# Optimization experiments

Measured on AMD Instinct MI355X. Metric: run time of the kernel, lower is better.

The kernel has to match this reference:

```python
import jax, jax.numpy as jnp
import numpy as np

TEMPERATURE = 0.2
NUM_CLASSES = 80  # background label == NUM_CLASSES
M, K, B = 8192, 128, 60


def setup_inputs() -> dict:
    key = jax.random.key(0)
    k1, k2, k3 = jax.random.split(key, 3)
    feats = jax.random.normal(k1, (M, K), dtype=jnp.float32)
    feats = feats / jnp.linalg.norm(feats, axis=-1, keepdims=True)
    protos = jax.random.normal(k2, (B, K), dtype=jnp.float32)
    protos = protos / jnp.linalg.norm(protos, axis=-1, keepdims=True)
    labels = jax.random.randint(k3, (M,), 0, NUM_CLASSES + 1)  # NUM_CLASSES == bg
    proto_labels = jnp.arange(B, dtype=jnp.int64 if jax.config.read('jax_enable_x64') else jnp.int32)
    return {"features": feats, "labels": labels, "protos": protos, "proto_labels": proto_labels}


def reference(features, labels, protos, proto_labels):
    # masked (fixed-shape) formulation of the original boolean-gather code
    fg = labels != NUM_CLASSES                                   # [M]
    is_base = fg & jnp.any(labels[None, :] == proto_labels[:, None], axis=0)
    is_novel = fg & ~is_base
    nf = is_novel.astype(features.dtype)                         # [M] novel mask
    bf = is_base.astype(features.dtype)                          # [M] base mask
    numel = jnp.sum(fg).astype(features.dtype)

    sim = jnp.matmul(features, features.T) / TEMPERATURE          # [M,M]
    pk = jnp.matmul(features, protos.T) / TEMPERATURE             # [M,B]
    exp_sim = jnp.exp(sim)                                        # [M,M]
    eye = jnp.eye(features.shape[0], dtype=features.dtype)
    offdiag = (1.0 - eye)

    # ---- novel branch: rows i with is_novel[i] ----
    # denom: sum over novel j != i of exp(sim) + sum over protos of RAW pk (faithful to source)
    exp_nn_sum = jnp.sum(exp_sim * nf[None, :] * offdiag, axis=1)  # [M]
    denom_n = exp_nn_sum + jnp.sum(pk, axis=1)                     # [M]
    log_prob = sim - jnp.log(denom_n)[:, None]
    # novel_label_mask in source is elementwise labels==labels -> all True
    n_novel = jnp.sum(nf)
    cnt = jnp.maximum(n_novel - 1.0, 1.0)                          # per-row positive count
    per_row_novel = -jnp.sum(log_prob * nf[None, :] * offdiag, axis=1) / cnt
    loss_novel = jnp.sum(per_row_novel * nf)
    loss_novel = jnp.where(n_novel > 1.0, loss_novel, 0.0)

    # ---- base branch: rows i with is_base[i] ----
    safe_lab = jnp.clip(labels, 0, protos.shape[0] - 1)
    pi = jnp.einsum('nc,nc->n', features, protos[safe_lab]) / TEMPERATURE  # [M]
    denom_b = jnp.sum(exp_sim * nf[None, :], axis=1) + jnp.sum(jnp.exp(pk), axis=1)
    loss_base = jnp.sum(bf * -(pi - jnp.log(denom_b)))
    loss_base = jnp.where(jnp.any(is_base), loss_base, 0.0)

    return (loss_novel + loss_base) / numel
```

## Files before the change

kernel.cpp:

```cpp
#include <hip/hip_runtime.h>
#include <math.h>

#define NCLS 80
#define KDIM 128
#define INV_T 5.0f
#define AST 136
#define BST 72

typedef __attribute__((ext_vector_type(4))) float  floatx4;
typedef __attribute__((ext_vector_type(8))) short  short8;

__device__ inline unsigned short f2bf(float x) {
    unsigned int u = __float_as_uint(x);
    u += 0x7fffu + ((u >> 16) & 1u);
    return (unsigned short)(u >> 16);
}
__device__ inline ushort4 pack4(float4 v) {
    ushort4 r; r.x = f2bf(v.x); r.y = f2bf(v.y); r.z = f2bf(v.z); r.w = f2bf(v.w);
    return r;
}

__global__ __launch_bounds__(256) void setup_kernel(
    const int* __restrict__ labels, int M, int B,
    int* __restrict__ novel_idx, int* __restrict__ counters,
    float* __restrict__ S1, float* __restrict__ T1,
    float* __restrict__ PKr, float* __restrict__ EK, float* __restrict__ out)
{
    int i = blockIdx.x * 256 + threadIdx.x;
    if (i == 0) out[0] = 0.f;
    if (i >= M) return;
    S1[i] = 0.f; T1[i] = 0.f; PKr[i] = 0.f; EK[i] = 0.f;
    int lab = labels[i];
    bool fg  = (lab != NCLS);
    bool isb = fg && (lab >= 0) && (lab < B);
    bool isn = fg && !isb;
    if (isn) { int p = atomicAdd(&counters[0], 1); novel_idx[p] = i; }
    if (fg)  atomicAdd(&counters[1], 1);
    if (isb) atomicAdd(&counters[2], 1);
}

__global__ __launch_bounds__(256, 2) void gemm_kernel(
    const float* __restrict__ feats, const float* __restrict__ protos,
    const int* __restrict__ novel_idx, const int* __restrict__ counters,
    int M, int B,
    float* __restrict__ S1, float* __restrict__ T1,
    float* __restrict__ PKr, float* __restrict__ EK)
{
    __shared__ unsigned short As[128 * AST];
    __shared__ unsigned short Bs[128 * BST];
    __shared__ int nidx[128];

    const int Nn = counters[0];
    const int ntiles = (Nn + 127) >> 7;
    const int ct = blockIdx.x >> 6;
    const int rt = blockIdx.x & 63;
    if (ct > ntiles) return;
    const bool isproto = (ct == ntiles);
    const int row0 = rt * 128;
    const int tid = threadIdx.x;

    {
        const float4* f4 = (const float4*)(feats + (size_t)row0 * KDIM);
        #pragma unroll
        for (int p = 0; p < 16; ++p) {
            int chunk = p * 256 + tid;
            int r = chunk >> 5, kc = chunk & 31;
            float4 v = f4[r * 32 + kc];
            *(ushort4*)&As[r * AST + kc * 4] = pack4(v);
        }
    }

    const int wave = tid >> 6;
    const int lane = tid & 63;
    const int lr   = lane & 15;
    const int quad = lane >> 4;
    const int wrow = (wave >> 1) * 64;
    const int wcol = (wave & 1) * 64;

    floatx4 acc[4][4];
    #pragma unroll
    for (int r = 0; r < 4; ++r)
        #pragma unroll
        for (int c = 0; c < 4; ++c)
            acc[r][c] = (floatx4){0.f, 0.f, 0.f, 0.f};

    for (int h = 0; h < 2; ++h) {
        if (h) __syncthreads();
        #pragma unroll
        for (int p = 0; p < 8; ++p) {
            int chunk = p * 256 + tid;
            int r = chunk >> 4, kc = chunk & 15;
            float4 v = make_float4(0.f, 0.f, 0.f, 0.f);
            if (isproto) {
                if (r < B) v = *(const float4*)(protos + (size_t)r * KDIM + h * 64 + kc * 4);
            } else {
                int jg = ct * 128 + r;
                if (jg < Nn) {
                    int nid = novel_idx[jg];
                    v = *(const float4*)(feats + (size_t)nid * KDIM + h * 64 + kc * 4);
                }
            }
            *(ushort4*)&Bs[r * BST + kc * 4] = pack4(v);
        }
        if (h == 0 && tid < 128) {
            int nid = -1;
            if (isproto) { if (tid < B) nid = tid; }
            else { int jg = ct * 128 + tid; if (jg < Nn) nid = novel_idx[jg]; }
            nidx[tid] = nid;
        }
        __syncthreads();
        #pragma unroll
        for (int ks = 0; ks < 2; ++ks) {
            short8 a[4], b[4];
            #pragma unroll
            for (int r = 0; r < 4; ++r)
                a[r] = *(const short8*)&As[(wrow + r * 16 + lr) * AST + h * 64 + ks * 32 + quad * 8];
            #pragma unroll
            for (int c = 0; c < 4; ++c)
                b[c] = *(const short8*)&Bs[(wcol + c * 16 + lr) * BST + ks * 32 + quad * 8];
            #pragma unroll
            for (int r = 0; r < 4; ++r)
                #pragma unroll
                for (int c = 0; c < 4; ++c)
                    acc[r][c] = __builtin_amdgcn_mfma_f32_16x16x32_bf16(
                        a[r], b[c], acc[r][c], 0, 0, 0);
        }
    }

    int ncol[4];
    #pragma unroll
    for (int c = 0; c < 4; ++c) ncol[c] = nidx[wcol + c * 16 + lr];

    #pragma unroll
    for (int r = 0; r < 4; ++r) {
        int ibase = row0 + wrow + r * 16 + quad * 4;
        #pragma unroll
        for (int reg = 0; reg < 4; ++reg) {
            int irow = ibase + reg;
            float se = 0.f, sr = 0.f;
            #pragma unroll
            for (int c = 0; c < 4; ++c) {
                float sim = acc[r][c][reg] * INV_T;
                bool valid = (ncol[c] >= 0) && (isproto || ncol[c] != irow);
                if (valid) { se += __expf(sim); sr += sim; }
            }
            #pragma unroll
            for (int off = 1; off < 16; off <<= 1) {
                se += __shfl_xor(se, off);
                sr += __shfl_xor(sr, off);
            }
            if (lr == 0) {
                if (isproto) { atomicAdd(&EK[irow], se); atomicAdd(&PKr[irow], sr); }
                else         { atomicAdd(&S1[irow], se); atomicAdd(&T1[irow], sr); }
            }
        }
    }
}

__global__ __launch_bounds__(256) void finalize_kernel(
    const float* __restrict__ feats, const float* __restrict__ protos,
    const int* __restrict__ labels,
    const float* __restrict__ S1, const float* __restrict__ T1,
    const float* __restrict__ PKr, const float* __restrict__ EK,
    const int* __restrict__ counters, int M, int B, float* __restrict__ out)
{
    __shared__ float part[16];
    const int tid  = threadIdx.x;
    const int rloc = tid >> 4;
    const int q    = tid & 15;
    const int row  = blockIdx.x * 16 + rloc;
    const int rs   = min(row, M - 1);

    const int Nn = counters[0], numel = counters[1], nbase = counters[2];

    int lab = labels[rs];
    bool fg  = (lab != NCLS);
    bool isb = fg && (lab >= 0) && (lab < B);
    bool isn = fg && !isb;
    int  sl  = min(max(lab, 0), B - 1);

    float d = 0.f;
    #pragma unroll
    for (int j = 0; j < 8; ++j) {
        int k = q + j * 16;
        d += feats[(size_t)rs * KDIM + k] * protos[(size_t)sl * KDIM + k];
    }
    #pragma unroll
    for (int off = 1; off < 16; off <<= 1) d += __shfl_xor(d, off);

    if (q == 0) {
        float loss = 0.f;
        if (row < M) {
            if (isn && Nn > 1) {
                float cnt = (float)(Nn - 1);
                float dn  = S1[rs] + PKr[rs];
                loss = -(T1[rs] - cnt * logf(dn)) / cnt;
            } else if (isb && nbase > 0) {
                float pi = d * INV_T;
                float db = S1[rs] + EK[rs];
                loss = -(pi - logf(db));
            }
        }
        part[rloc] = loss;
    }
    __syncthreads();
    if (tid == 0) {
        float s = 0.f;
        #pragma unroll
        for (int r = 0; r < 16; ++r) s += part[r];
        atomicAdd(out, s / (float)numel);
    }
}

extern "C" void kernel_launch(void* const* d_in, const int* in_sizes, int n_in,
                              void* d_out, int out_size, void* d_ws, size_t ws_size,
                              hipStream_t stream)
{
    const float* feats  = (const float*)d_in[0];
    const int*   labels = (const int*)d_in[1];
    const float* protos = (const float*)d_in[2];

    const int M = in_sizes[1];
    const int B = in_sizes[3];

    char* ws = (char*)d_ws;
    int*   counters  = (int*)ws;
    float* S1  = (float*)(ws + 64);
    float* T1  = S1 + M;
    float* PKr = T1 + M;
    float* EK  = PKr + M;
    int*   novel_idx = (int*)(EK + M);

    hipMemsetAsync(counters, 0, 64, stream);

    setup_kernel<<<(M + 255) / 256, 256, 0, stream>>>(
        labels, M, B, novel_idx, counters, S1, T1, PKr, EK, (float*)d_out);

    int rowTiles = (M + 127) / 128;
    int maxct    = (M + 127) / 128;
    gemm_kernel<<<rowTiles * (maxct + 1), 256, 0, stream>>>(
        feats, protos, novel_idx, counters, M, B, S1, T1, PKr, EK);

    finalize_kernel<<<(M + 15) / 16, 256, 0, stream>>>(
        feats, protos, labels, S1, T1, PKr, EK, counters, M, B, (float*)d_out);
}
```

Measured before the change: 107.5 us.

## Pre-convert features to bf16 once and stream tiles via direct global-to-LDS loads

The setup kernel now converts all feature and prototype rows to bf16 once into workspace, including a zero pad row used for out-of-range novel columns. The GEMM kernel then fills its A and B tiles with global_load_lds 16-byte transfers into an XOR-swizzled LDS layout instead of per-block fp32 loads and conversions. The full K=128 tile is loaded at once with a single barrier. This removes repeated fp32 reads and conversions that every column tile did for the same rows. In exchange it adds a bf16 copy to workspace, a larger LDS footprint (64KB), and a dependency on the swizzle matching the lane-address layout of global_load_lds.

```diff
diff --git a/kernel.cpp b/kernel.cpp
--- a/kernel.cpp
+++ b/kernel.cpp
@@ -4,8 +4,6 @@
 #define NCLS 80
 #define KDIM 128
 #define INV_T 5.0f
-#define AST 136
-#define BST 72
 
 typedef __attribute__((ext_vector_type(4))) float  floatx4;
 typedef __attribute__((ext_vector_type(8))) short  short8;
@@ -15,39 +13,69 @@
     u += 0x7fffu + ((u >> 16) & 1u);
     return (unsigned short)(u >> 16);
 }
-__device__ inline ushort4 pack4(float4 v) {
-    ushort4 r; r.x = f2bf(v.x); r.y = f2bf(v.y); r.z = f2bf(v.z); r.w = f2bf(v.w);
-    return r;
+__device__ inline short8 pack8(float4 a, float4 b) {
+    short8 o;
+    o[0] = (short)f2bf(a.x); o[1] = (short)f2bf(a.y);
+    o[2] = (short)f2bf(a.z); o[3] = (short)f2bf(a.w);
+    o[4] = (short)f2bf(b.x); o[5] = (short)f2bf(b.y);
+    o[6] = (short)f2bf(b.z); o[7] = (short)f2bf(b.w);
+    return o;
+}
+__device__ inline void g2lds16(const void* g, void* l) {
+    __builtin_amdgcn_global_load_lds(
+        (const __attribute__((address_space(1))) void*)g,
+        (__attribute__((address_space(3))) void*)l, 16, 0, 0);
 }
 
 __global__ __launch_bounds__(256) void setup_kernel(
-    const int* __restrict__ labels, int M, int B,
+    const float* __restrict__ feats, const int* __restrict__ labels,
+    const float* __restrict__ protos, int M, int B,
     int* __restrict__ novel_idx, int* __restrict__ counters,
     float* __restrict__ S1, float* __restrict__ T1,
-    float* __restrict__ PKr, float* __restrict__ EK, float* __restrict__ out)
-{
-    int i = blockIdx.x * 256 + threadIdx.x;
+    float* __restrict__ PKr, float* __restrict__ EK, float* __restrict__ out,
+    unsigned short* __restrict__ Fb, unsigned short* __restrict__ Pb)
+{
+    const int i = blockIdx.x * 256 + threadIdx.x;
+    const int T = gridDim.x * 256;
     if (i == 0) out[0] = 0.f;
-    if (i >= M) return;
-    S1[i] = 0.f; T1[i] = 0.f; PKr[i] = 0.f; EK[i] = 0.f;
-    int lab = labels[i];
-    bool fg  = (lab != NCLS);
-    bool isb = fg && (lab >= 0) && (lab < B);
-    bool isn = fg && !isb;
-    if (isn) { int p = atomicAdd(&counters[0], 1); novel_idx[p] = i; }
-    if (fg)  atomicAdd(&counters[1], 1);
-    if (isb) atomicAdd(&counters[2], 1);
+    if (i < M) {
+        S1[i] = 0.f; T1[i] = 0.f; PKr[i] = 0.f; EK[i] = 0.f;
+        int lab = labels[i];
+        bool fg  = (lab != NCLS);
+        bool isb = fg && (lab >= 0) && (lab < B);
+        bool isn = fg && !isb;
+        if (isn) { int p = atomicAdd(&counters[0], 1); novel_idx[p] = i; }
+        if (fg)  atomicAdd(&counters[1], 1);
+        if (isb) atomicAdd(&counters[2], 1);
+    }
+    const int nch = (M + 1) * (KDIM / 8);
+    for (int ch = i; ch < nch; ch += T) {
+        short8 o = (short8)0;
+        if (ch < M * (KDIM / 8)) {
+            const float4* f4 = (const float4*)feats + (size_t)ch * 2;
+            o = pack8(f4[0], f4[1]);
+        }
+        *(short8*)&Fb[(size_t)ch * 8] = o;
+    }
+    for (int ch = i; ch < 128 * (KDIM / 8); ch += T) {
+        short8 o = (short8)0;
+        if (ch < B * (KDIM / 8)) {
+            const float4* f4 = (const float4*)protos + (size_t)ch * 2;
+            o = pack8(f4[0], f4[1]);
+        }
+        *(short8*)&Pb[(size_t)ch * 8] = o;
+    }
 }
 
 __global__ __launch_bounds__(256, 2) void gemm_kernel(
-    const float* __restrict__ feats, const float* __restrict__ protos,
+    const unsigned short* __restrict__ Fb, const unsigned short* __restrict__ Pb,
     const int* __restrict__ novel_idx, const int* __restrict__ counters,
     int M, int B,
     float* __restrict__ S1, float* __restrict__ T1,
     float* __restrict__ PKr, float* __restrict__ EK)
 {
-    __shared__ unsigned short As[128 * AST];
-    __shared__ unsigned short Bs[128 * BST];
+    __shared__ unsigned short As[128 * 128];
+    __shared__ unsigned short Bs[128 * 128];
     __shared__ int nidx[128];
 
     const int Nn = counters[0];
@@ -58,17 +86,43 @@
     const bool isproto = (ct == ntiles);
     const int row0 = rt * 128;
     const int tid = threadIdx.x;
+    const int wbase = tid & ~63;
 
     {
-        const float4* f4 = (const float4*)(feats + (size_t)row0 * KDIM);
-        #pragma unroll
-        for (int p = 0; p < 16; ++p) {
-            int chunk = p * 256 + tid;
-            int r = chunk >> 5, kc = chunk & 31;
-            float4 v = f4[r * 32 + kc];
-            *(ushort4*)&As[r * AST + kc * 4] = pack4(v);
-        }
-    }
+        const unsigned short* a0 = Fb + (size_t)row0 * KDIM;
+        #pragma unroll
+        for (int p = 0; p < 8; ++p) {
+            int Lc = p * 256 + tid;
+            int r = Lc >> 4, c = Lc & 15;
+            int cs = c ^ (r & 15);
+            g2lds16(a0 + r * KDIM + cs * 8, As + (size_t)(p * 256 + wbase) * 8);
+        }
+    }
+    {
+        #pragma unroll
+        for (int p = 0; p < 8; ++p) {
+            int Lc = p * 256 + tid;
+            int r = Lc >> 4, c = Lc & 15;
+            int cs = c ^ (r & 15);
+            const unsigned short* base;
+            int nid;
+            if (isproto) { base = Pb; nid = r; }
+            else {
+                base = Fb;
+                int jg = ct * 128 + r;
+                nid = (jg < Nn) ? novel_idx[jg] : M;
+            }
+            g2lds16(base + (size_t)nid * KDIM + cs * 8,
+                    Bs + (size_t)(p * 256 + wbase) * 8);
+        }
+    }
+    if (tid < 128) {
+        int nid = -1;
+        if (isproto) { if (tid < B) nid = tid; }
+        else { int jg = ct * 128 + tid; if (jg < Nn) nid = novel_idx[jg]; }
+        nidx[tid] = nid;
+    }
+    __syncthreads();
 
     const int wave = tid >> 6;
     const int lane = tid & 63;
@@ -84,47 +138,27 @@
         for (int c = 0; c < 4; ++c)
             acc[r][c] = (floatx4){0.f, 0.f, 0.f, 0.f};
 
-    for (int h = 0; h < 2; ++h) {
-        if (h) __syncthreads();
-        #pragma unroll
-        for (int p = 0; p < 8; ++p) {
-            int chunk = p * 256 + tid;
-            int r = chunk >> 4, kc = chunk & 15;
-            float4 v = make_float4(0.f, 0.f, 0.f, 0.f);
-            if (isproto) {
-                if (r < B) v = *(const float4*)(protos + (size_t)r * KDIM + h * 64 + kc * 4);
-            } else {
-                int jg = ct * 128 + r;
-                if (jg < Nn) {
-                    int nid = novel_idx[jg];
-                    v = *(const float4*)(feats + (size_t)nid * KDIM + h * 64 + kc * 4);
-                }
-            }
-            *(ushort4*)&Bs[r * BST + kc * 4] = pack4(v);
-        }
-        if (h == 0 && tid < 128) {
-            int nid = -1;
-            if (isproto) { if (tid < B) nid = tid; }
-            else { int jg = ct * 128 + tid; if (jg < Nn) nid = novel_idx[jg]; }
-            nidx[tid] = nid;
-        }
-        __syncthreads();
-        #pragma unroll
-        for (int ks = 0; ks < 2; ++ks) {
-            short8 a[4], b[4];
-            #pragma unroll
-            for (int r = 0; r < 4; ++r)
-                a[r] = *(const short8*)&As[(wrow + r * 16 + lr) * AST + h * 64 + ks * 32 + quad * 8];
+    #pragma unroll
+    for (int ks = 0; ks < 4; ++ks) {
+        short8 a[4], b[4];
+        #pragma unroll
+        for (int r = 0; r < 4; ++r) {
+            int row = wrow + r * 16 + lr;
+            int phys = (ks * 4 + quad) ^ lr;
+            a[r] = *(const short8*)&As[row * KDIM + phys * 8];
+        }
+        #pragma unroll
+        for (int c = 0; c < 4; ++c) {
+            int row = wcol + c * 16 + lr;
+            int phys = (ks * 4 + quad) ^ lr;
+            b[c] = *(const short8*)&Bs[row * KDIM + phys * 8];
+        }
+        #pragma unroll
+        for (int r = 0; r < 4; ++r)
             #pragma unroll
             for (int c = 0; c < 4; ++c)
-                b[c] = *(const short8*)&Bs[(wcol + c * 16 + lr) * BST + ks * 32 + quad * 8];
-            #pragma unroll
-            for (int r = 0; r < 4; ++r)
-                #pragma unroll
-                for (int c = 0; c < 4; ++c)
-                    acc[r][c] = __builtin_amdgcn_mfma_f32_16x16x32_bf16(
-                        a[r], b[c], acc[r][c], 0, 0, 0);
-        }
+                acc[r][c] = __builtin_amdgcn_mfma_f32_16x16x32_bf16(
+                    a[r], b[c], acc[r][c], 0, 0, 0);
     }
 
     int ncol[4];
@@ -230,16 +264,19 @@
     float* PKr = T1 + M;
     float* EK  = PKr + M;
     int*   novel_idx = (int*)(EK + M);
+    unsigned short* Fb = (unsigned short*)(novel_idx + M);
+    unsigned short* Pb = Fb + (size_t)(M + 1) * KDIM;
 
     hipMemsetAsync(counters, 0, 64, stream);
 
-    setup_kernel<<<(M + 255) / 256, 256, 0, stream>>>(
-        labels, M, B, novel_idx, counters, S1, T1, PKr, EK, (float*)d_out);
+    setup_kernel<<<256, 256, 0, stream>>>(
+        feats, labels, protos, M, B, novel_idx, counters,
+        S1, T1, PKr, EK, (float*)d_out, Fb, Pb);
 
     int rowTiles = (M + 127) / 128;
     int maxct    = (M + 127) / 128;
     gemm_kernel<<<rowTiles * (maxct + 1), 256, 0, stream>>>(
-        feats, protos, novel_idx, counters, M, B, S1, T1, PKr, EK);
+        Fb, Pb, novel_idx, counters, M, B, S1, T1, PKr, EK);
 
     finalize_kernel<<<(M + 15) / 16, 256, 0, stream>>>(
         feats, protos, labels, S1, T1, PKr, EK, counters, M, B, (float*)d_out);
```

After: 104.1 us. 1.03x faster.
